# Optimization experiments

Measured on AMD Instinct MI355X. Metric: run time of the kernel, lower is better.

Reference implementation:

```python
import jax, jax.numpy as jnp
import numpy as np

B, T = 32, 512
C = 1024          # hidden_units
H, D = 16, 64     # n_head, head_size (n_attn = H*D = 1024)
NATTN = H * D
R = D // 2        # rotary_ndims = int(head_size * 0.5) = 32
NITEMS = 100001   # item_num + 1 (padding_idx = 0)
NUSERS = 1000


def _rotate_half(x):
    x1, x2 = jnp.split(x, 2, axis=-1)
    return jnp.concatenate([-x2, x1], axis=-1)


def _rope_cos_sin(t_len):
    # RotaryEmbedding(dim=R): inv_freq over arange(0, R, 2)
    inv_freq = 1.0 / (10000.0 ** (jnp.arange(0, R, 2, dtype=jnp.float32) / R))
    t = jnp.arange(t_len, dtype=jnp.float32)
    freqs = jnp.einsum('i,j->ij', t, inv_freq)          # [T, R/2]
    emb = jnp.concatenate([freqs, freqs], axis=-1)      # [T, R]
    return jnp.cos(emb), jnp.sin(emb)


def _mha_rotary(log_seqs, item_emb, Wq, bq, Wk, bk, Wv, bv, Wo, bo):
    x = item_emb[log_seqs]                               # [B,T,C]
    q = (x @ Wq + bq).reshape(B, T, H, D).transpose(0, 2, 1, 3)  # [B,H,T,D]
    k = (x @ Wk + bk).reshape(B, T, H, D).transpose(0, 2, 1, 3)
    v = (x @ Wv + bv).reshape(B, T, H, D).transpose(0, 2, 1, 3)
    # partial rotary on first R dims
    q_rot, q_pass = q[..., :R], q[..., R:]
    k_rot, k_pass = k[..., :R], k[..., R:]
    cos, sin = _rope_cos_sin(T)                          # [T,R] broadcast over B,H
    q_rot = q_rot * cos + _rotate_half(q_rot) * sin
    k_rot = k_rot * cos + _rotate_half(k_rot) * sin
    q = jnp.concatenate([q_rot, q_pass], axis=-1)
    k = jnp.concatenate([k_rot, k_pass], axis=-1)
    att = jnp.einsum('bhqd,bhkd->bhqk', q, k) * (1.0 / np.sqrt(D))
    causal = jnp.tril(jnp.ones((T, T), dtype=bool))
    att = jnp.where(causal, att, -jnp.inf)
    att = jax.nn.softmax(att, axis=-1)
    o = jnp.einsum('bhqk,bhkd->bhqd', att, v)            # [B,H,T,D]
    o = o.transpose(0, 2, 1, 3).reshape(B, T, NATTN)
    return o @ Wo + bo                                   # [B,T,C]


def setup_inputs() -> dict:
    key = jax.random.key(0)
    ks = jax.random.split(key, 12)
    s = 0.02
    item_emb = (jax.random.normal(ks[0], (NITEMS, C), jnp.float32) * s).at[0].set(0.0)
    Wq = jax.random.normal(ks[1], (C, NATTN), jnp.float32) * s
    Wk = jax.random.normal(ks[2], (C, NATTN), jnp.float32) * s
    Wv = jax.random.normal(ks[3], (C, NATTN), jnp.float32) * s
    Wo = jax.random.normal(ks[4], (NATTN, C), jnp.float32) * s
    bq = jnp.zeros((NATTN,), jnp.float32)
    bk = jnp.zeros((NATTN,), jnp.float32)
    bv = jnp.zeros((NATTN,), jnp.float32)
    bo = jnp.zeros((C,), jnp.float32)
    user_ids = jax.random.randint(ks[5], (B,), 0, NUSERS)
    log_seqs = jax.random.randint(ks[6], (B, T), 0, NITEMS)
    pos_seqs = jax.random.randint(ks[7], (B, T), 0, NITEMS)
    neg_seqs = jax.random.randint(ks[8], (B, T), 0, NITEMS)
    return {"user_ids": user_ids, "log_seqs": log_seqs, "pos_seqs": pos_seqs,
            "neg_seqs": neg_seqs, "item_emb": item_emb,
            "Wq": Wq, "bq": bq, "Wk": Wk, "bk": bk, "Wv": Wv, "bv": bv,
            "Wo": Wo, "bo": bo}


def reference(user_ids, log_seqs, pos_seqs, neg_seqs, item_emb,
              Wq, bq, Wk, bk, Wv, bv, Wo, bo):
    log_feats = _mha_rotary(log_seqs, item_emb, Wq, bq, Wk, bk, Wv, bv, Wo, bo)
    pos_embs = item_emb[pos_seqs]                        # [B,T,C]
    neg_embs = item_emb[neg_seqs]
    pos_logits = log_feats * pos_embs                    # elementwise (no sum, as in source)
    neg_logits = (log_feats * neg_embs).sum(axis=-1)     # [B,T]
    return (pos_logits, neg_logits)
```

## Files before the change

kernel.cpp:

```cpp
#include <hip/hip_runtime.h>
#include <hip/hip_bf16.h>

#define BB   32
#define TT   512
#define CC   1024
#define HH   16
#define DD   64
#define BT   (BB*TT)
#define SZROW 1024

typedef __bf16 bf16x8 __attribute__((ext_vector_type(8)));
typedef float  f32x4  __attribute__((ext_vector_type(4)));

#define GLDS16(g, s)                                                        \
    __builtin_amdgcn_global_load_lds(                                       \
        (const __attribute__((address_space(1))) void*)(g),                 \
        (__attribute__((address_space(3))) void*)(s), 16, 0, 0)

__device__ __forceinline__ __bf16 tobf(float x) {
    union { float f; uint32_t u; } v; v.f = x;
    uint32_t r = (v.u + 0x7fffu + ((v.u >> 16) & 1u)) >> 16;
    union { unsigned short s; __bf16 b; } o; o.s = (unsigned short)r;
    return o.b;
}
__device__ __forceinline__ uint32_t pk2bf(float a, float b) {
    union { __bf16 h; unsigned short s; } x, y;
    x.h = tobf(a); y.h = tobf(b);
    return ((uint32_t)y.s << 16) | (uint32_t)x.s;
}

__global__ __launch_bounds__(256) void k_trig(float2* __restrict__ trig)
{
    const int idx = blockIdx.x * 256 + threadIdx.x;
    const int t = idx >> 4, i = idx & 15;
    const float inv = __expf(-(float)i * 0.5756462732485115f);
    float s, c;
    sincosf((float)t * inv, &s, &c);
    trig[idx] = make_float2(c, s);
}

__global__ __launch_bounds__(256) void k_cast(const float* __restrict__ src,
                                              const int*   __restrict__ idx,
                                              __bf16*      __restrict__ dst)
{
    const int t   = blockIdx.x * 256 + threadIdx.x;
    const int row = t >> 7;
    const int c   = (t & 127) << 3;
    const int srow = idx ? idx[row] : row;
    const float* s = src + (size_t)srow * SZROW + c;
    float4 a = *(const float4*)s;
    float4 b = *(const float4*)(s + 4);
    __bf16 o[8] = { tobf(a.x), tobf(a.y), tobf(a.z), tobf(a.w),
                    tobf(b.x), tobf(b.y), tobf(b.z), tobf(b.w) };
    *(uint4*)(dst + (size_t)row * SZROW + c) = *(const uint4*)o;
}

__global__ __launch_bounds__(256) void k_wt(const float* __restrict__ W0,
                                            const float* __restrict__ W1,
                                            const float* __restrict__ W2,
                                            const float* __restrict__ W3,
                                            __bf16*      __restrict__ Wt)
{
    __shared__ float tile[32][33];
    const int z = blockIdx.z;
    const float* W = (z == 0) ? W0 : (z == 1) ? W1 : (z == 2) ? W2 : W3;
    __bf16* dst = Wt + (size_t)z * SZROW * SZROW;

    const int n0 = blockIdx.x * 32, k0 = blockIdx.y * 32;
    const int t = threadIdx.x;
    const int r = t >> 3, c4 = (t & 7) << 2;
    float4 v = *(const float4*)&W[(size_t)(k0 + r) * SZROW + n0 + c4];
    tile[r][c4 + 0] = v.x; tile[r][c4 + 1] = v.y;
    tile[r][c4 + 2] = v.z; tile[r][c4 + 3] = v.w;
    __syncthreads();
    __bf16 o[4] = { tobf(tile[c4 + 0][r]), tobf(tile[c4 + 1][r]),
                    tobf(tile[c4 + 2][r]), tobf(tile[c4 + 3][r]) };
    *(uint2*)&dst[(size_t)(n0 + r) * SZROW + k0 + c4] = *(const uint2*)o;
}

__device__ __forceinline__ void gemm_main(const __bf16* __restrict__ A,
                                          const __bf16* __restrict__ Wt,
                                          int m0, int n0,
                                          f32x4 (&acc)[4][4])
{
    __shared__ __bf16 As[4][128][8];
    __shared__ __bf16 Bs[4][128][8];

    const int tid = threadIdx.x;
    const int lane = tid & 63;
    const int wid  = tid >> 6;
    const int wm   = (wid >> 1) << 6;
    const int wn   = (wid & 1) << 6;

    const int lr = lane & 15;
    const int lg = lane >> 4;

    const __bf16* aA0 = A  + (size_t)(m0 + lane)      * 1024 + (wid << 3);
    const __bf16* aA1 = A  + (size_t)(m0 + 64 + lane) * 1024 + (wid << 3);
    const __bf16* aB0 = Wt + (size_t)(n0 + lane)      * 1024 + (wid << 3);
    const __bf16* aB1 = Wt + (size_t)(n0 + 64 + lane) * 1024 + (wid << 3);

    #pragma unroll
    for (int m = 0; m < 4; ++m)
        #pragma unroll
        for (int n = 0; n < 4; ++n) {
            acc[m][n][0] = 0.f; acc[m][n][1] = 0.f;
            acc[m][n][2] = 0.f; acc[m][n][3] = 0.f;
        }

    for (int kt = 0; kt < 1024; kt += 32) {
        __syncthreads();
        GLDS16(aA0 + kt, &As[wid][ 0][0]);
        GLDS16(aA1 + kt, &As[wid][64][0]);
        GLDS16(aB0 + kt, &Bs[wid][ 0][0]);
        GLDS16(aB1 + kt, &Bs[wid][64][0]);
        __syncthreads();

        bf16x8 af[4], bfr[4];
        #pragma unroll
        for (int m = 0; m < 4; ++m)
            af[m] = *(const bf16x8*)&As[lg][wm + (m << 4) + lr][0];
        #pragma unroll
        for (int n = 0; n < 4; ++n)
            bfr[n] = *(const bf16x8*)&Bs[lg][wn + (n << 4) + lr][0];

        #pragma unroll
        for (int m = 0; m < 4; ++m)
            #pragma unroll
            for (int n = 0; n < 4; ++n)
                acc[m][n] = __builtin_amdgcn_mfma_f32_16x16x32_bf16(
                                af[m], bfr[n], acc[m][n], 0, 0, 0);
    }
}

__global__ __launch_bounds__(256) void k_qkv(const __bf16* __restrict__ Abf,
                                             const __bf16* __restrict__ Wtq,
                                             const __bf16* __restrict__ Wtk,
                                             const __bf16* __restrict__ Wtv,
                                             const float* __restrict__ bq,
                                             const float* __restrict__ bk,
                                             const float* __restrict__ bv,
                                             const float2* __restrict__ trig,
                                             __bf16* __restrict__ Qbh,
                                             __bf16* __restrict__ Kbh,
                                             __bf16* __restrict__ Vtb)
{
    const int z = blockIdx.z;
    const __bf16* W    = (z == 0) ? Wtq : (z == 1) ? Wtk : Wtv;
    const float*  bias = (z == 0) ? bq  : (z == 1) ? bk  : bv;

    const int m0 = blockIdx.y * 128, n0 = blockIdx.x * 128;
    f32x4 acc[4][4];
    gemm_main(Abf, W, m0, n0, acc);

    const int tid = threadIdx.x;
    const int lane = tid & 63, wid = tid >> 6;
    const int wm = (wid >> 1) << 6, wn = (wid & 1) << 6;
    const int lr = lane & 15, lg = lane >> 4;
    const int h = (n0 + wn) >> 6;

    float bb4[4];
    #pragma unroll
    for (int n = 0; n < 4; ++n) bb4[n] = bias[n0 + wn + (n << 4) + lr];

    if (z < 2) {
        __bf16* dst = (z == 0) ? Qbh : Kbh;
        #pragma unroll
        for (int m = 0; m < 4; ++m) {
            const int rbase = m0 + wm + (m << 4) + (lg << 2);
            const int b  = rbase >> 9;
            const int t0 = rbase & 511;
            const size_t obase = ((size_t)(b * 16 + h)) * 512 * 64;
            #pragma unroll
            for (int i = 0; i < 4; ++i) {
                const int t = t0 + i;
                const float2 cs = trig[(t << 4) + lr];
                const float a0 = acc[m][0][i] + bb4[0];
                const float a1 = acc[m][1][i] + bb4[1];
                const float a2 = acc[m][2][i] + bb4[2];
                const float a3 = acc[m][3][i] + bb4[3];
                const size_t o = obase + (size_t)t * 64;
                dst[o + lr]      = tobf(a0 * cs.x - a1 * cs.y);
                dst[o + lr + 16] = tobf(a1 * cs.x + a0 * cs.y);
                dst[o + lr + 32] = tobf(a2);
                dst[o + lr + 48] = tobf(a3);
            }
        }
    } else {
        #pragma unroll
        for (int m = 0; m < 4; ++m) {
            const int rbase = m0 + wm + (m << 4) + (lg << 2);
            const int b  = rbase >> 9;
            const int t0 = rbase & 511;
            #pragma unroll
            for (int n = 0; n < 4; ++n) {
                const int d = (n << 4) + lr;
                __bf16 pk[4] = { tobf(acc[m][n][0] + bb4[n]),
                                 tobf(acc[m][n][1] + bb4[n]),
                                 tobf(acc[m][n][2] + bb4[n]),
                                 tobf(acc[m][n][3] + bb4[n]) };
                *(uint2*)&Vtb[((size_t)((b * 16 + h) * 64 + d)) * 512 + t0] =
                    *(const uint2*)pk;
            }
        }
    }
}

__global__ __launch_bounds__(256) void k_proj(const __bf16* __restrict__ Abf,
                                              const __bf16* __restrict__ Wt,
                                              const float* __restrict__ bias,
                                              float* __restrict__ out)
{
    const int m0 = blockIdx.y * 128, n0 = blockIdx.x * 128;
    f32x4 acc[4][4];
    gemm_main(Abf, Wt, m0, n0, acc);

    const int tid = threadIdx.x;
    const int lane = tid & 63, wid = tid >> 6;
    const int wm = (wid >> 1) << 6, wn = (wid & 1) << 6;
    const int lr = lane & 15, lg = lane >> 4;

    #pragma unroll
    for (int n = 0; n < 4; ++n) {
        const int col = n0 + wn + (n << 4) + lr;
        const float bv = bias[col];
        #pragma unroll
        for (int m = 0; m < 4; ++m) {
            const int rbase = m0 + wm + (m << 4) + (lg << 2);
            #pragma unroll
            for (int i = 0; i < 4; ++i)
                out[(size_t)(rbase + i) * SZROW + col] = acc[m][n][i] + bv;
        }
    }
}

__global__ __launch_bounds__(256) void k_attn(const __bf16* __restrict__ Qbh,
                                              const __bf16* __restrict__ Kbh,
                                              const __bf16* __restrict__ Vtb,
                                              __bf16* __restrict__ Obf)
{
    __shared__ __bf16 Kl[64][64];
    __shared__ __bf16 Vl[64][64];
    __shared__ __bf16 Pl[4][16][64];

    const int tid = threadIdx.x;
    const int lane = tid & 63, w = tid >> 6;
    const int qt = blockIdx.x, bh = blockIdx.y;
    const int b = bh >> 4, h = bh & 15;
    const int lr = lane & 15, lg = lane >> 4;
    const int sw = lr & 7;

    const int qrow = (qt << 6) + (w << 4) + lr;
    const __bf16* qsrc = Qbh + ((size_t)bh * 512 + qrow) * 64 + (lg << 3);
    const bf16x8 qf0 = *(const bf16x8*)(qsrc);
    const bf16x8 qf1 = *(const bf16x8*)(qsrc + 32);

    const int srow  = (w << 4) + (lane >> 3);
    const int lslot = (lane & 7) ^ (srow & 7);
    const __bf16* ksrc = Kbh + ((size_t)bh * 512 + srow) * 64 + (lslot << 3);
    const __bf16* vsrc = Vtb + ((size_t)bh * 64 + srow) * 512 + (lslot << 3);

    f32x4 oAcc[4];
    #pragma unroll
    for (int n = 0; n < 4; ++n) {
        oAcc[n][0] = 0.f; oAcc[n][1] = 0.f; oAcc[n][2] = 0.f; oAcc[n][3] = 0.f;
    }
    float m_run = -3.0e38f, l_run = 0.0f;

    for (int kt = 0; kt <= qt; ++kt) {
        __syncthreads();
        GLDS16(ksrc + (size_t)((kt << 6) + 0) * 64, &Kl[(w << 4) + 0][0]);
        GLDS16(ksrc + (size_t)((kt << 6) + 8) * 64, &Kl[(w << 4) + 8][0]);
        GLDS16(vsrc + (kt << 6),                    &Vl[(w << 4) + 0][0]);
        GLDS16(vsrc + (kt << 6) + 8 * 512,          &Vl[(w << 4) + 8][0]);
        __syncthreads();

        const bool diag = (kt == qt);
        const int mmax = diag ? w : 3;

        f32x4 sT[4];
        #pragma unroll
        for (int m = 0; m < 4; ++m) {
            sT[m][0] = 0.f; sT[m][1] = 0.f; sT[m][2] = 0.f; sT[m][3] = 0.f;
        }
        for (int m = 0; m <= mmax; ++m) {
            const int row = (m << 4) + lr;
            bf16x8 kf0 = *(const bf16x8*)&Kl[row][(lg ^ sw) << 3];
            sT[m] = __builtin_amdgcn_mfma_f32_16x16x32_bf16(kf0, qf0, sT[m], 0, 0, 0);
            bf16x8 kf1 = *(const bf16x8*)&Kl[row][((4 + lg) ^ sw) << 3];
            sT[m] = __builtin_amdgcn_mfma_f32_16x16x32_bf16(kf1, qf1, sT[m], 0, 0, 0);
        }

        float pv[4][4];
        float pmax = -3.0e38f;
        #pragma unroll
        for (int m = 0; m < 4; ++m)
            #pragma unroll
            for (int i = 0; i < 4; ++i) {
                float s = (m <= mmax) ? sT[m][i] * 0.125f : -3.0e38f;
                if (diag && ((m << 4) + (lg << 2) + i > (w << 4) + lr)) s = -3.0e38f;
                pv[m][i] = s;
                pmax = fmaxf(pmax, s);
            }
        pmax = fmaxf(pmax, __shfl_xor(pmax, 16));
        pmax = fmaxf(pmax, __shfl_xor(pmax, 32));
        const float mnew = fmaxf(m_run, pmax);
        const float alpha = __expf(m_run - mnew);
        float psum = 0.0f;
        #pragma unroll
        for (int m = 0; m < 4; ++m)
            #pragma unroll
            for (int i = 0; i < 4; ++i) {
                const float p = __expf(pv[m][i] - mnew);
                pv[m][i] = p;
                psum += p;
            }
        psum += __shfl_xor(psum, 16);
        psum += __shfl_xor(psum, 32);
        l_run = l_run * alpha + psum;
        m_run = mnew;

        #pragma unroll
        for (int m = 0; m < 4; ++m)
            #pragma unroll
            for (int ip = 0; ip < 4; ip += 2) {
                const int key = (m << 4) + (lg << 2) + ip;
                const int slot = key >> 3;
                __bf16* dst = &Pl[w][lr][((slot ^ sw) << 3) + (key & 7)];
                *(uint32_t*)dst = pk2bf(pv[m][ip], pv[m][ip + 1]);
            }

        float av[4];
        #pragma unroll
        for (int i = 0; i < 4; ++i) av[i] = __shfl(alpha, (lg << 2) + i);
        #pragma unroll
        for (int n = 0; n < 4; ++n)
            #pragma unroll
            for (int i = 0; i < 4; ++i) oAcc[n][i] *= av[i];

        #pragma unroll
        for (int step = 0; step < 2; ++step) {
            const int sl = ((step << 2) + lg) ^ sw;
            bf16x8 paf = *(const bf16x8*)&Pl[w][lr][sl << 3];
            #pragma unroll
            for (int n = 0; n < 4; ++n) {
                bf16x8 vf = *(const bf16x8*)&Vl[(n << 4) + lr][sl << 3];
                oAcc[n] = __builtin_amdgcn_mfma_f32_16x16x32_bf16(paf, vf, oAcc[n], 0, 0, 0);
            }
        }
    }

    float linv[4];
    #pragma unroll
    for (int i = 0; i < 4; ++i) linv[i] = 1.0f / __shfl(l_run, (lg << 2) + i);
    #pragma unroll
    for (int n = 0; n < 4; ++n) {
        const int d = (n << 4) + lr;
        #pragma unroll
        for (int i = 0; i < 4; ++i) {
            const int t = (qt << 6) + (w << 4) + (lg << 2) + i;
            Obf[((size_t)(b * 512 + t)) * SZROW + (h << 6) + d] =
                tobf(oAcc[n][i] * linv[i]);
        }
    }
}

__global__ __launch_bounds__(256) void k_epi(const float* __restrict__ LF,
                                             const float* __restrict__ emb,
                                             const int*   __restrict__ pos,
                                             const int*   __restrict__ neg,
                                             float* __restrict__ out)
{
    __shared__ float red[4];
    const int r = blockIdx.x;
    const int tid = threadIdx.x;
    const float* lf = LF  + (size_t)r * SZROW;
    const float* pe = emb + (size_t)pos[r] * SZROW;
    const float* ne = emb + (size_t)neg[r] * SZROW;
    float* po = out + (size_t)r * SZROW;

    const int c = tid << 2;
    float4 l4 = *(const float4*)&lf[c];
    float4 p4 = *(const float4*)&pe[c];
    float4 n4 = *(const float4*)&ne[c];
    float4 o4;
    o4.x = l4.x * p4.x; o4.y = l4.y * p4.y; o4.z = l4.z * p4.z; o4.w = l4.w * p4.w;
    *(float4*)&po[c] = o4;

    float nsum = l4.x*n4.x + l4.y*n4.y + l4.z*n4.z + l4.w*n4.w;
    #pragma unroll
    for (int off = 32; off > 0; off >>= 1) nsum += __shfl_down(nsum, off);
    if ((tid & 63) == 0) red[tid >> 6] = nsum;
    __syncthreads();
    if (tid == 0) out[(size_t)BT * SZROW + r] = red[0] + red[1] + red[2] + red[3];
}

extern "C" void kernel_launch(void* const* d_in, const int* in_sizes, int n_in,
                              void* d_out, int out_size, void* d_ws, size_t ws_size,
                              hipStream_t stream)
{
    const int*   log_seqs = (const int*)  d_in[1];
    const int*   pos_seqs = (const int*)  d_in[2];
    const int*   neg_seqs = (const int*)  d_in[3];
    const float* item_emb = (const float*)d_in[4];
    const float* Wq = (const float*)d_in[5];
    const float* bq = (const float*)d_in[6];
    const float* Wk = (const float*)d_in[7];
    const float* bk = (const float*)d_in[8];
    const float* Wv = (const float*)d_in[9];
    const float* bv = (const float*)d_in[10];
    const float* Wo = (const float*)d_in[11];
    const float* bo = (const float*)d_in[12];

    char* wsb = (char*)d_ws;
    const size_t MB32 = (size_t)32 << 20;
    __bf16* Abf = (__bf16*)(wsb);
    __bf16* Qbh = (__bf16*)(wsb + 1 * MB32);
    __bf16* Kbh = (__bf16*)(wsb + 2 * MB32);
    __bf16* Vtb = (__bf16*)(wsb + 3 * MB32);
    __bf16* Obf = (__bf16*)(wsb + 4 * MB32);
    __bf16* Wt  = (__bf16*)(wsb + 5 * MB32);
    __bf16* Wt0 = Wt;
    __bf16* Wt1 = Wt0 + (size_t)SZROW * SZROW;
    __bf16* Wt2 = Wt1 + (size_t)SZROW * SZROW;
    __bf16* Wt3 = Wt2 + (size_t)SZROW * SZROW;
    float2* trig = (float2*)(wsb + 5 * MB32 + 4 * ((size_t)SZROW * SZROW * 2));
    float*  LF  = (float*)(wsb);
    float* out = (float*)d_out;

    k_trig<<<32, 256, 0, stream>>>(trig);
    k_wt<<<dim3(32, 32, 4), 256, 0, stream>>>(Wq, Wk, Wv, Wo, Wt);

    k_cast<<<BT * 128 / 256, 256, 0, stream>>>(item_emb, log_seqs, Abf);

    k_qkv<<<dim3(8, 128, 3), 256, 0, stream>>>(Abf, Wt0, Wt1, Wt2, bq, bk, bv,
                                               trig, Qbh, Kbh, Vtb);

    k_attn<<<dim3(8, 512), 256, 0, stream>>>(Qbh, Kbh, Vtb, Obf);

    k_proj<<<dim3(8, 128, 1), 256, 0, stream>>>(Obf, Wt3, bo, LF);

    k_epi<<<BT, 256, 0, stream>>>(LF, item_emb, pos_seqs, neg_seqs, out);
}
```

Measured before the change: 934.9 us.

## Fuse output projection with logits epilogue and remap block order for cache reuse

The output projection GEMM now computes the positive and negative logits directly in its epilogue. This removes the fp32 intermediate write and re-read and the separate epilogue kernel. Negative-logit row sums are combined with shuffles and atomicAdd into an output zeroed by a new small kernel. Block indices in the QKV, projection and attention kernels are remapped to group tiles for L2 reuse, and the attention diagonal tile skips a PV step for the half-empty warps. In exchange, the epilogue reads the embedding scattered per element instead of as float4, and the atomics make the summation order nondeterministic.

```diff
diff --git a/kernel.cpp b/kernel.cpp
--- a/kernel.cpp
+++ b/kernel.cpp
@@ -39,6 +39,11 @@
     trig[idx] = make_float2(c, s);
 }
 
+__global__ __launch_bounds__(256) void k_zero(float* __restrict__ p)
+{
+    p[blockIdx.x * 256 + threadIdx.x] = 0.0f;
+}
+
 __global__ __launch_bounds__(256) void k_cast(const float* __restrict__ src,
                                               const int*   __restrict__ idx,
                                               __bf16*      __restrict__ dst)
@@ -46,7 +51,7 @@
     const int t   = blockIdx.x * 256 + threadIdx.x;
     const int row = t >> 7;
     const int c   = (t & 127) << 3;
-    const int srow = idx ? idx[row] : row;
+    const int srow = idx[row];
     const float* s = src + (size_t)srow * SZROW + c;
     float4 a = *(const float4*)s;
     float4 b = *(const float4*)(s + 4);
@@ -149,7 +154,11 @@
     const __bf16* W    = (z == 0) ? Wtq : (z == 1) ? Wtk : Wtv;
     const float*  bias = (z == 0) ? bq  : (z == 1) ? bk  : bv;
 
-    const int m0 = blockIdx.y * 128, n0 = blockIdx.x * 128;
+    const int lin = blockIdx.x + (blockIdx.y << 3);
+    const int m_blk = (lin & 7) + (((lin >> 3) & 15) << 3);
+    const int n_blk = lin >> 7;
+    const int m0 = m_blk * 128, n0 = n_blk * 128;
+
     f32x4 acc[4][4];
     gemm_main(Abf, W, m0, n0, acc);
 
@@ -206,30 +215,54 @@
     }
 }
 
-__global__ __launch_bounds__(256) void k_proj(const __bf16* __restrict__ Abf,
-                                              const __bf16* __restrict__ Wt,
-                                              const float* __restrict__ bias,
-                                              float* __restrict__ out)
-{
-    const int m0 = blockIdx.y * 128, n0 = blockIdx.x * 128;
+__global__ __launch_bounds__(256) void k_projepi(const __bf16* __restrict__ Obf,
+                                                 const __bf16* __restrict__ Wt,
+                                                 const float* __restrict__ bias,
+                                                 const float* __restrict__ emb,
+                                                 const int*   __restrict__ pos,
+                                                 const int*   __restrict__ neg,
+                                                 float* __restrict__ out)
+{
+    const int lin = blockIdx.x + (blockIdx.y << 3);
+    const int m_blk = (lin & 7) + (((lin >> 3) & 15) << 3);
+    const int n_blk = lin >> 7;
+    const int m0 = m_blk * 128, n0 = n_blk * 128;
+
     f32x4 acc[4][4];
-    gemm_main(Abf, Wt, m0, n0, acc);
+    gemm_main(Obf, Wt, m0, n0, acc);
 
     const int tid = threadIdx.x;
     const int lane = tid & 63, wid = tid >> 6;
     const int wm = (wid >> 1) << 6, wn = (wid & 1) << 6;
     const int lr = lane & 15, lg = lane >> 4;
 
-    #pragma unroll
-    for (int n = 0; n < 4; ++n) {
-        const int col = n0 + wn + (n << 4) + lr;
-        const float bv = bias[col];
-        #pragma unroll
-        for (int m = 0; m < 4; ++m) {
-            const int rbase = m0 + wm + (m << 4) + (lg << 2);
-            #pragma unroll
-            for (int i = 0; i < 4; ++i)
-                out[(size_t)(rbase + i) * SZROW + col] = acc[m][n][i] + bv;
+    float bb4[4];
+    #pragma unroll
+    for (int n = 0; n < 4; ++n) bb4[n] = bias[n0 + wn + (n << 4) + lr];
+
+    float* negout = out + (size_t)BT * SZROW;
+
+    #pragma unroll
+    for (int m = 0; m < 4; ++m) {
+        const int rbase = m0 + wm + (m << 4) + (lg << 2);
+        #pragma unroll
+        for (int i = 0; i < 4; ++i) {
+            const int row = rbase + i;
+            const size_t pbase = (size_t)pos[row] * SZROW;
+            const size_t nbase = (size_t)neg[row] * SZROW;
+            float nsum = 0.0f;
+            #pragma unroll
+            for (int n = 0; n < 4; ++n) {
+                const int col = n0 + wn + (n << 4) + lr;
+                const float lf = acc[m][n][i] + bb4[n];
+                out[(size_t)row * SZROW + col] = lf * emb[pbase + col];
+                nsum = fmaf(lf, emb[nbase + col], nsum);
+            }
+            nsum += __shfl_xor(nsum, 1);
+            nsum += __shfl_xor(nsum, 2);
+            nsum += __shfl_xor(nsum, 4);
+            nsum += __shfl_xor(nsum, 8);
+            if (lr == 0) atomicAdd(&negout[row], nsum);
         }
     }
 }
@@ -245,7 +278,9 @@
 
     const int tid = threadIdx.x;
     const int lane = tid & 63, w = tid >> 6;
-    const int qt = blockIdx.x, bh = blockIdx.y;
+    const int lin = blockIdx.x + (blockIdx.y << 3);
+    const int qt = (lin >> 3) & 7;
+    const int bh = (lin & 7) + ((lin >> 6) << 3);
     const int b = bh >> 4, h = bh & 15;
     const int lr = lane & 15, lg = lane >> 4;
     const int sw = lr & 7;
@@ -338,8 +373,8 @@
             #pragma unroll
             for (int i = 0; i < 4; ++i) oAcc[n][i] *= av[i];
 
-        #pragma unroll
-        for (int step = 0; step < 2; ++step) {
+        const int nstep = (diag && w < 2) ? 1 : 2;
+        for (int step = 0; step < nstep; ++step) {
             const int sl = ((step << 2) + lg) ^ sw;
             bf16x8 paf = *(const bf16x8*)&Pl[w][lr][sl << 3];
             #pragma unroll
@@ -363,36 +398,6 @@
                 tobf(oAcc[n][i] * linv[i]);
         }
     }
-}
-
-__global__ __launch_bounds__(256) void k_epi(const float* __restrict__ LF,
-                                             const float* __restrict__ emb,
-                                             const int*   __restrict__ pos,
-                                             const int*   __restrict__ neg,
-                                             float* __restrict__ out)
-{
-    __shared__ float red[4];
-    const int r = blockIdx.x;
-    const int tid = threadIdx.x;
-    const float* lf = LF  + (size_t)r * SZROW;
-    const float* pe = emb + (size_t)pos[r] * SZROW;
-    const float* ne = emb + (size_t)neg[r] * SZROW;
-    float* po = out + (size_t)r * SZROW;
-
-    const int c = tid << 2;
-    float4 l4 = *(const float4*)&lf[c];
-    float4 p4 = *(const float4*)&pe[c];
-    float4 n4 = *(const float4*)&ne[c];
-    float4 o4;
-    o4.x = l4.x * p4.x; o4.y = l4.y * p4.y; o4.z = l4.z * p4.z; o4.w = l4.w * p4.w;
-    *(float4*)&po[c] = o4;
-
-    float nsum = l4.x*n4.x + l4.y*n4.y + l4.z*n4.z + l4.w*n4.w;
-    #pragma unroll
-    for (int off = 32; off > 0; off >>= 1) nsum += __shfl_down(nsum, off);
-    if ((tid & 63) == 0) red[tid >> 6] = nsum;
-    __syncthreads();
-    if (tid == 0) out[(size_t)BT * SZROW + r] = red[0] + red[1] + red[2] + red[3];
 }
 
 extern "C" void kernel_launch(void* const* d_in, const int* in_sizes, int n_in,
@@ -425,10 +430,10 @@
     __bf16* Wt2 = Wt1 + (size_t)SZROW * SZROW;
     __bf16* Wt3 = Wt2 + (size_t)SZROW * SZROW;
     float2* trig = (float2*)(wsb + 5 * MB32 + 4 * ((size_t)SZROW * SZROW * 2));
-    float*  LF  = (float*)(wsb);
     float* out = (float*)d_out;
 
     k_trig<<<32, 256, 0, stream>>>(trig);
+    k_zero<<<BT / 256, 256, 0, stream>>>(out + (size_t)BT * SZROW);
     k_wt<<<dim3(32, 32, 4), 256, 0, stream>>>(Wq, Wk, Wv, Wo, Wt);
 
     k_cast<<<BT * 128 / 256, 256, 0, stream>>>(item_emb, log_seqs, Abf);
@@ -438,7 +443,6 @@
 
     k_attn<<<dim3(8, 512), 256, 0, stream>>>(Qbh, Kbh, Vtb, Obf);
 
-    k_proj<<<dim3(8, 128, 1), 256, 0, stream>>>(Obf, Wt3, bo, LF);
-
-    k_epi<<<BT, 256, 0, stream>>>(LF, item_emb, pos_seqs, neg_seqs, out);
-}
+    k_projepi<<<dim3(8, 128), 256, 0, stream>>>(Obf, Wt3, bo, item_emb,
+                                                pos_seqs, neg_seqs, out);
+}
```

Measured after the change: 914.4 us. 1.02x faster.
